# Kernel optimization log

Hardware: AMD Instinct MI355X
Metric: run time of the kernel (lower is better)

## Reference

```python
import jax, jax.numpy as jnp
import numpy as np

B, CIN, COUT, H, W = 4, 64, 64, 64, 64
DI, DS, DR, K = 2 * COUT, 16, COUT // 16, 4   # d_inner, d_state, dt_rank, scan dirs
EPS = 1e-5


def _conv(x, w, b, groups=1):
    y = jax.lax.conv_general_dilated(x, w, (1, 1), 'SAME', feature_group_count=groups,
                                     dimension_numbers=('NCHW', 'OIHW', 'NCHW'))
    return y + b[None, :, None, None]


def _inorm(x):  # InstanceNorm2d, no affine
    m = x.mean(axis=(2, 3), keepdims=True)
    v = x.var(axis=(2, 3), keepdims=True)
    return (x - m) * jax.lax.rsqrt(v + EPS)


def _lrelu(x):
    return jnp.where(x >= 0, x, 0.2 * x)


def _ln(x, g, b):
    m = x.mean(-1, keepdims=True)
    v = x.var(-1, keepdims=True)
    return (x - m) * jax.lax.rsqrt(v + EPS) * g + b


def _ss2d(x, in_proj_w, dw_w, dw_b, x_proj_w, dt_proj_w, dt_proj_b,
          A_logs, Ds, out_norm_g, out_norm_b, out_proj_w):
    # x: (b, h, w, c)
    b, h, w, c = x.shape
    L = h * w
    xz = jnp.einsum('bhwc,ec->bhwe', x, in_proj_w)      # (b,h,w,2*DI)
    xin, z = jnp.split(xz, 2, axis=-1)
    xin = xin.transpose(0, 3, 1, 2)                      # (b,DI,h,w)
    xin = _conv(xin, dw_w, dw_b, groups=DI)              # depthwise 3x3
    xin = jax.nn.silu(xin)
    # 4-direction scans: row-major, col-major, and their reverses
    x_hw = xin.reshape(b, DI, L)
    x_wh = xin.transpose(0, 1, 3, 2).reshape(b, DI, L)
    xs = jnp.stack([x_hw, x_wh, jnp.flip(x_hw, -1), jnp.flip(x_wh, -1)], axis=1)  # (b,K,DI,L)
    x_dbl = jnp.einsum('bkdl,kcd->bkcl', xs, x_proj_w)   # c = DR + 2*DS
    dts, Bs, Cs = jnp.split(x_dbl, [DR, DR + DS], axis=2)
    dt = jax.nn.softplus(jnp.einsum('bkrl,kdr->bkdl', dts, dt_proj_w)
                         + dt_proj_b[None, :, :, None])  # (b,K,DI,L)
    A = -jnp.exp(A_logs)                                  # (K,DI,DS)

    def step(hst, inp):
        dt_t, B_t, C_t, u_t = inp  # (b,K,DI),(b,K,DS),(b,K,DS),(b,K,DI)
        hst = hst * jnp.exp(dt_t[..., None] * A[None]) + (dt_t * u_t)[..., None] * B_t[:, :, None, :]
        y = jnp.einsum('bkdn,bkn->bkd', hst, C_t)
        return hst, y

    h0 = jnp.zeros((b, K, DI, DS), xs.dtype)
    scan_in = (dt.transpose(3, 0, 1, 2), Bs.transpose(3, 0, 1, 2),
               Cs.transpose(3, 0, 1, 2), xs.transpose(3, 0, 1, 2))
    _, ys = jax.lax.scan(step, h0, scan_in)               # (L,b,K,DI)
    ys = ys.transpose(1, 2, 3, 0) + Ds[None, :, :, None] * xs  # (b,K,DI,L)
    # undo the 4 traversal orders and sum
    y0 = ys[:, 0]
    y1 = ys[:, 1].reshape(b, DI, w, h).transpose(0, 1, 3, 2).reshape(b, DI, L)
    y2 = jnp.flip(ys[:, 2], -1)
    y3 = jnp.flip(ys[:, 3], -1).reshape(b, DI, w, h).transpose(0, 1, 3, 2).reshape(b, DI, L)
    y = (y0 + y1 + y2 + y3).transpose(0, 2, 1)            # (b,L,DI)
    y = _ln(y, out_norm_g, out_norm_b)
    y = y * jax.nn.silu(z.reshape(b, L, DI))
    out = jnp.einsum('bld,cd->blc', y, out_proj_w)        # (b,L,c)
    return out.reshape(b, h, w, c)


def _mamba(x, cf_w, cf_b, ln_g, ln_b, in_proj_w, dw_w, dw_b, x_proj_w,
           dt_proj_w, dt_proj_b, A_logs, Ds, out_norm_g, out_norm_b,
           out_proj_w, skip_scale, cb_w, cb_b):
    x1 = _conv(x, cf_w, cf_b)                 # shallow feature conv
    xs = x1.transpose(0, 2, 3, 1)             # (b,h,w,c)
    xs = xs * skip_scale + _ss2d(_ln(xs, ln_g, ln_b), in_proj_w, dw_w, dw_b,
                                 x_proj_w, dt_proj_w, dt_proj_b, A_logs, Ds,
                                 out_norm_g, out_norm_b, out_proj_w)
    res = xs.transpose(0, 3, 1, 2)
    return _conv(res, cb_w, cb_b) + x1        # conv_after_body + residual


def reference(x, conv1_w, conv1_b, conv2_w, conv2_b, cf_w, cf_b, ln_g, ln_b,
              in_proj_w, dw_w, dw_b, x_proj_w, dt_proj_w, dt_proj_b, A_logs,
              Ds, out_norm_g, out_norm_b, out_proj_w, skip_scale, cb_w, cb_b):
    out = _lrelu(_inorm(_conv(x, conv1_w, conv1_b)))
    out = _conv(out, conv2_w, conv2_b)
    out = _mamba(out, cf_w, cf_b, ln_g, ln_b, in_proj_w, dw_w, dw_b, x_proj_w,
                 dt_proj_w, dt_proj_b, A_logs, Ds, out_norm_g, out_norm_b,
                 out_proj_w, skip_scale, cb_w, cb_b)
    return _lrelu(_inorm(out))


def setup_inputs() -> dict:
    key = jax.random.key(0)
    ks = jax.random.split(key, 12)
    n = lambda k, shape, scale: jax.random.normal(k, shape, jnp.float32) * scale
    p = {}
    p['x'] = jax.random.normal(ks[0], (B, CIN, H, W), jnp.float32)
    p['conv1_w'] = n(ks[1], (COUT, CIN, 3, 3), (CIN * 9) ** -0.5)
    p['conv1_b'] = jnp.zeros((COUT,))
    p['conv2_w'] = n(ks[2], (COUT, COUT, 3, 3), (COUT * 9) ** -0.5)
    p['conv2_b'] = jnp.zeros((COUT,))
    p['cf_w'] = n(ks[3], (COUT, COUT, 3, 3), (COUT * 9) ** -0.5)
    p['cf_b'] = jnp.zeros((COUT,))
    p['ln_g'] = jnp.ones((COUT,))
    p['ln_b'] = jnp.zeros((COUT,))
    p['in_proj_w'] = n(ks[4], (2 * DI, COUT), COUT ** -0.5)
    p['dw_w'] = n(ks[5], (DI, 1, 3, 3), 1.0 / 3.0)
    p['dw_b'] = jnp.zeros((DI,))
    p['x_proj_w'] = n(ks[6], (K, DR + 2 * DS, DI), DI ** -0.5)
    p['dt_proj_w'] = n(ks[7], (K, DI, DR), DR ** -0.5)
    p['dt_proj_b'] = jnp.full((K, DI), float(np.log(np.expm1(0.01))), jnp.float32)
    p['A_logs'] = jnp.log(jnp.tile(jnp.arange(1., DS + 1., dtype=jnp.float32), (K, DI, 1)))
    p['Ds'] = jnp.ones((K, DI))
    p['out_norm_g'] = jnp.ones((DI,))
    p['out_norm_b'] = jnp.zeros((DI,))
    p['out_proj_w'] = n(ks[8], (COUT, DI), DI ** -0.5)
    p['skip_scale'] = jnp.ones(())
    p['cb_w'] = n(ks[9], (COUT, COUT, 3, 3), (COUT * 9) ** -0.5)
    p['cb_b'] = jnp.zeros((COUT,))
    return p
```

## Files before the change

kernel.cpp:

```cpp
#include <hip/hip_runtime.h>
#include <hip/hip_bf16.h>


typedef __attribute__((ext_vector_type(8))) short bf16x8;
typedef __attribute__((ext_vector_type(8))) unsigned short u16x8;
typedef __attribute__((ext_vector_type(4))) float f32x4;
typedef unsigned short u16;

static __device__ __forceinline__ short f2bf(float f)
{
    unsigned u = __float_as_uint(f);
    unsigned r = u + 0x7FFFu + ((u >> 16) & 1u);
    return (short)(r >> 16);
}
static __device__ __forceinline__ float b2f(u16 s)
{
    return __uint_as_float((unsigned)s << 16);
}

static __device__ __forceinline__ float softplus_f(float s)
{
    return (s > 15.f) ? s : __logf(1.f + __expf(s));
}

static __device__ __forceinline__ float dpp_sum16(float x)
{
    x += __int_as_float(__builtin_amdgcn_update_dpp(
        0, __float_as_int(x), 0xB1, 0xF, 0xF, true));
    x += __int_as_float(__builtin_amdgcn_update_dpp(
        0, __float_as_int(x), 0x4E, 0xF, 0xF, true));
    x += __int_as_float(__builtin_amdgcn_update_dpp(
        0, __float_as_int(x), 0x141, 0xF, 0xF, true));
    x += __int_as_float(__builtin_amdgcn_update_dpp(
        0, __float_as_int(x), 0x140, 0xF, 0xF, true));
    return x;
}

__global__ __launch_bounds__(256) void wconv_k(const float* __restrict__ w1,
    const float* __restrict__ w2, const float* __restrict__ w3,
    const float* __restrict__ w4, const float* __restrict__ ipw,
    const float* __restrict__ xpw, short* __restrict__ wbf,
    short* __restrict__ wxp)
{
    const int idx = blockIdx.x * 256 + threadIdx.x;
    if (idx < 147456) {
        const int c = idx / 36864, rem = idx % 36864;
        const int tap = rem >> 12, r2 = rem & 4095;
        const int co = r2 >> 6, ci = r2 & 63;
        const float* src = (c == 0) ? w1 : (c == 1) ? w2 : (c == 2) ? w3 : w4;
        wbf[idx] = f2bf(src[(co * 64 + ci) * 9 + tap]);
    } else if (idx < 163840) {
        const int i2 = idx - 147456;
        wbf[idx] = f2bf(ipw[i2]);
    } else {
        const int i3 = idx - 163840;
        const int src = i3 / 10240, r = i3 % 10240;
        const int cc = r >> 7, dd = r & 127;
        float v = 0.f;
        if (cc < 72) {
            const int k = src + ((cc >= 36) ? 2 : 0);
            const int c = (cc >= 36) ? (cc - 36) : cc;
            v = xpw[((size_t)(k * 36 + c)) * 128 + dd];
        }
        wxp[i3] = f2bf(v);
    }
}

__global__ __launch_bounds__(256) void conv3x3_mfma_k(const float* __restrict__ in,
    const short* __restrict__ wtap, const float* __restrict__ bias,
    const float* __restrict__ addsrc, const float* __restrict__ instats,
    float* __restrict__ outstats, float* __restrict__ out)
{
    const int bh = blockIdx.x;
    const int b = bh >> 6, h = bh & 63;
    const int t = threadIdx.x;
    __shared__ __align__(16) short lin[3 * 66 * 72];
    {
        const int ci = t >> 2, w16 = (t & 3) * 16;
        float mu = 0.f, rstd = 1.f;
        if (instats) {
            const float S1 = instats[(b << 6) + ci];
            const float S2 = instats[256 + (b << 6) + ci];
            mu = S1 * (1.f / 4096.f);
            rstd = rsqrtf(S2 * (1.f / 4096.f) - mu * mu + 1e-5f);
        }
#pragma unroll
        for (int r = 0; r < 3; ++r) {
            const int hh = h - 1 + r;
            const bool ok = (hh >= 0 && hh < 64);
            const float* src = in + ((size_t)(b * 64 + ci) * 64 + (ok ? hh : 0)) * 64 + w16;
#pragma unroll
            for (int q = 0; q < 4; ++q) {
                float4 v = make_float4(0.f, 0.f, 0.f, 0.f);
                if (ok) {
                    v = *(const float4*)(src + q * 4);
                    if (instats) {
#define NRM(E) { float nv = (v.E - mu) * rstd; v.E = (nv >= 0.f) ? nv : 0.2f * nv; }
                        NRM(x) NRM(y) NRM(z) NRM(w)
#undef NRM
                    }
                }
                const int wb = w16 + q * 4;
                lin[(r * 66 + wb + 1) * 72 + ci] = f2bf(v.x);
                lin[(r * 66 + wb + 2) * 72 + ci] = f2bf(v.y);
                lin[(r * 66 + wb + 3) * 72 + ci] = f2bf(v.z);
                lin[(r * 66 + wb + 4) * 72 + ci] = f2bf(v.w);
            }
        }
        if (t < 216) {
            const int r3 = t / 72, rem = t % 72;
            const int colp = (rem >= 36) ? 65 : 0, ci2 = rem % 36;
            ((int*)lin)[(r3 * 66 + colp) * 36 + ci2] = 0;
        }
    }
    __syncthreads();
    const int lane = t & 63, ct = t >> 6;
    const int n16 = lane & 15, quad = lane >> 4;
    f32x4 acc0 = {0.f, 0.f, 0.f, 0.f};
    f32x4 acc1 = {0.f, 0.f, 0.f, 0.f};
    f32x4 acc2 = {0.f, 0.f, 0.f, 0.f};
    f32x4 acc3 = {0.f, 0.f, 0.f, 0.f};
#pragma unroll
    for (int tap = 0; tap < 9; ++tap) {
        const int dy = tap / 3, dx = tap % 3;
#pragma unroll
        for (int kh = 0; kh < 2; ++kh) {
            const int kk = kh * 32;
            const bf16x8 a = *(const bf16x8*)(wtap +
                ((size_t)tap * 64 + ct * 16 + n16) * 64 + kk + quad * 8);
            const int rb = (dy * 66 + n16 + dx) * 72 + kk + quad * 8;
            const bf16x8 b0 = *(const bf16x8*)&lin[rb + 0 * 16 * 72];
            const bf16x8 b1 = *(const bf16x8*)&lin[rb + 1 * 16 * 72];
            const bf16x8 b2 = *(const bf16x8*)&lin[rb + 2 * 16 * 72];
            const bf16x8 b3 = *(const bf16x8*)&lin[rb + 3 * 16 * 72];
            acc0 = __builtin_amdgcn_mfma_f32_16x16x32_bf16(a, b0, acc0, 0, 0, 0);
            acc1 = __builtin_amdgcn_mfma_f32_16x16x32_bf16(a, b1, acc1, 0, 0, 0);
            acc2 = __builtin_amdgcn_mfma_f32_16x16x32_bf16(a, b2, acc2, 0, 0, 0);
            acc3 = __builtin_amdgcn_mfma_f32_16x16x32_bf16(a, b3, acc3, 0, 0, 0);
        }
    }
#pragma unroll
    for (int r = 0; r < 4; ++r) {
        const int co = ct * 16 + quad * 4 + r;
        const float bv = bias[co];
        float* orow = out + ((size_t)(b * 64 + co) * 64 + h) * 64;
        float v0 = acc0[r] + bv, v1 = acc1[r] + bv, v2 = acc2[r] + bv, v3 = acc3[r] + bv;
        if (addsrc) {
            const float* arow = addsrc + ((size_t)(b * 64 + co) * 64 + h) * 64;
            v0 += arow[n16]; v1 += arow[16 + n16];
            v2 += arow[32 + n16]; v3 += arow[48 + n16];
        }
        if (outstats) {
            float ss = (v0 + v1) + (v2 + v3);
            float qq = fmaf(v0, v0, fmaf(v1, v1, fmaf(v2, v2, v3 * v3)));
            ss = dpp_sum16(ss);
            qq = dpp_sum16(qq);
            if (n16 == 0) {
                atomicAdd(&outstats[(b << 6) + co], ss);
                atomicAdd(&outstats[256 + (b << 6) + co], qq);
            }
        }
        orow[n16] = v0; orow[16 + n16] = v1;
        orow[32 + n16] = v2; orow[48 + n16] = v3;
    }
}

__global__ __launch_bounds__(256) void inorm_apply_k(const float* __restrict__ in,
    const float* __restrict__ stats, float* __restrict__ out)
{
    const int bc = blockIdx.x;
    const float S1 = stats[bc], S2 = stats[256 + bc];
    const float mu = S1 * (1.f / 4096.f);
    const float rstd = rsqrtf(S2 * (1.f / 4096.f) - mu * mu + 1e-5f);
    const float* row = in + (size_t)bc * 4096;
    float* orow = out + (size_t)bc * 4096;
    for (int i = threadIdx.x; i < 4096; i += 256) {
        float v = (row[i] - mu) * rstd;
        orow[i] = (v >= 0.f) ? v : 0.2f * v;
    }
}

__global__ __launch_bounds__(256) void ln_inproj_mfma_k(const float* __restrict__ x1,
    const float* __restrict__ g, const float* __restrict__ be,
    const short* __restrict__ wip, u16* __restrict__ xinrawD,
    float* __restrict__ z)
{
    const int bx = blockIdx.x;
    const int b = bx >> 7, l0 = (bx & 127) * 32;
    const int t = threadIdx.x;
    __shared__ __align__(16) short ltile[32 * 72];
    __shared__ float ztile[32 * 140];
    __shared__ __align__(16) u16 stile[32 * 136];
    {
        const int j = t & 31, gg = t >> 5;
        float xr[64];
        float s1 = 0.f, s2 = 0.f;
#pragma unroll
        for (int c = 0; c < 64; ++c) {
            const float v = x1[(b * 64 + c) * 4096 + l0 + j];
            xr[c] = v; s1 += v; s2 = fmaf(v, v, s2);
        }
        const float mu = s1 * (1.f / 64.f);
        const float var = s2 * (1.f / 64.f) - mu * mu;
        const float rstd = rsqrtf(var + 1e-5f);
#pragma unroll
        for (int i = 0; i < 8; ++i) {
            const int c = gg * 8 + i;
            ltile[j * 72 + c] = f2bf((xr[c] - mu) * rstd * g[c] + be[c]);
        }
    }
    __syncthreads();
    const int lane = t & 63, wv = t >> 6;
    const int n16 = lane & 15, quad = lane >> 4;
    f32x4 acc[4][2];
#pragma unroll
    for (int i = 0; i < 4; ++i)
#pragma unroll
        for (int p = 0; p < 2; ++p) acc[i][p] = (f32x4){0.f, 0.f, 0.f, 0.f};
#pragma unroll
    for (int i = 0; i < 4; ++i) {
        const int cot = wv * 4 + i;
#pragma unroll
        for (int kh = 0; kh < 2; ++kh) {
            const bf16x8 a = *(const bf16x8*)(wip +
                (size_t)(cot * 16 + n16) * 64 + kh * 32 + quad * 8);
#pragma unroll
            for (int p = 0; p < 2; ++p) {
                const bf16x8 bb = *(const bf16x8*)&ltile[
                    (p * 16 + n16) * 72 + kh * 32 + quad * 8];
                acc[i][p] = __builtin_amdgcn_mfma_f32_16x16x32_bf16(a, bb, acc[i][p], 0, 0, 0);
            }
        }
    }
#pragma unroll
    for (int i = 0; i < 4; ++i) {
        const int cot = wv * 4 + i;
#pragma unroll
        for (int p = 0; p < 2; ++p) {
            const int pos = p * 16 + n16;
#pragma unroll
            for (int r = 0; r < 4; ++r) {
                const int e = cot * 16 + quad * 4 + r;
                const float v = acc[i][p][r];
                if (e < 128) stile[pos * 136 + e] = (u16)f2bf(v);
                else ztile[pos * 140 + (e - 128)] = v;
            }
        }
    }
    __syncthreads();
    {
        const int pos = t >> 3, d0 = (t & 7) * 16;
        float* dst = z + ((size_t)(b * 4096 + l0 + pos)) * 128 + d0;
        const float* srcz = ztile + pos * 140 + d0;
#pragma unroll
        for (int q = 0; q < 4; ++q)
            *(float4*)(dst + q * 4) = *(const float4*)(srcz + q * 4);
        u16* dst2 = xinrawD + ((size_t)(b * 4096 + l0 + pos)) * 128 + d0;
        *(u16x8*)dst2 = *(const u16x8*)&stile[pos * 136 + d0];
        *(u16x8*)(dst2 + 8) = *(const u16x8*)&stile[pos * 136 + d0 + 8];
    }
}

__global__ __launch_bounds__(256) void dwconv_dT_k(const u16* __restrict__ in,
    const float* __restrict__ w, const float* __restrict__ bias,
    u16* __restrict__ xin_sD, u16* __restrict__ xin_TD)
{
    __shared__ float sw[1152];
    __shared__ float sb[128];
    for (int e = threadIdx.x; e < 1152; e += 256) sw[e] = w[e];
    if (threadIdx.x < 128) sb[threadIdx.x] = bias[threadIdx.x];
    __syncthreads();
    const int bx = blockIdx.x;
    const int b = bx >> 9, m0 = (bx & 511) * 8;
    const int t = threadIdx.x;
    const int d = t & 127, mloc = t >> 7;
    const u16* base = in + (size_t)b * 4096 * 128 + d;
    const float* wd = sw + d * 9;
    const float bv = sb[d];
#pragma unroll
    for (int i = 0; i < 4; ++i) {
        const int m = m0 + mloc + i * 2;
        const int hh = m >> 6, ww = m & 63;
        float acc = bv;
        const bool hm = hh > 0, hp = hh < 63, wm = ww > 0, wp = ww < 63;
        if (hm) {
            const u16* r = base + (m - 64) * 128;
            if (wm) acc = fmaf(b2f(r[-128]), wd[0], acc);
            acc = fmaf(b2f(r[0]), wd[1], acc);
            if (wp) acc = fmaf(b2f(r[128]), wd[2], acc);
        }
        {
            const u16* r = base + m * 128;
            if (wm) acc = fmaf(b2f(r[-128]), wd[3], acc);
            acc = fmaf(b2f(r[0]), wd[4], acc);
            if (wp) acc = fmaf(b2f(r[128]), wd[5], acc);
        }
        if (hp) {
            const u16* r = base + (m + 64) * 128;
            if (wm) acc = fmaf(b2f(r[-128]), wd[6], acc);
            acc = fmaf(b2f(r[0]), wd[7], acc);
            if (wp) acc = fmaf(b2f(r[128]), wd[8], acc);
        }
        const float val = acc / (1.f + __expf(-acc));
        const u16 bf = (u16)f2bf(val);
        xin_sD[((size_t)b * 4096 + m) * 128 + d] = bf;
        xin_TD[((size_t)b * 4096 + (ww * 64 + hh)) * 128 + d] = bf;
    }
}

__global__ __launch_bounds__(256) void xdbl_mfma_k(const u16* __restrict__ xin_sD,
    const u16* __restrict__ xin_TD, const short* __restrict__ wxp,
    float* __restrict__ xdbl_mc)
{
    const int bx = blockIdx.x;
    const int tile = bx & 63, src = (bx >> 6) & 1, b = bx >> 7;
    const int m0 = tile * 64;
    const int t = threadIdx.x;
    const int wv = t >> 6, lane = t & 63;
    const int n16 = lane & 15, quad = lane >> 4;
    const u16* srcp = (src ? xin_TD : xin_sD) + (size_t)b * 4096 * 128;
    const short* wb = wxp + (size_t)src * 80 * 128;
    f32x4 acc[5];
#pragma unroll
    for (int c = 0; c < 5; ++c) acc[c] = (f32x4){0.f, 0.f, 0.f, 0.f};
    const u16* brow = srcp + (size_t)(m0 + wv * 16 + n16) * 128 + quad * 8;
#pragma unroll
    for (int kc = 0; kc < 4; ++kc) {
        const bf16x8 bfrag = *(const bf16x8*)(brow + kc * 32);
#pragma unroll
        for (int ct = 0; ct < 5; ++ct) {
            const bf16x8 afrag = *(const bf16x8*)(wb +
                (size_t)(ct * 16 + n16) * 128 + kc * 32 + quad * 8);
            acc[ct] = __builtin_amdgcn_mfma_f32_16x16x32_bf16(afrag, bfrag, acc[ct], 0, 0, 0);
        }
    }
    __shared__ float sres[64 * 81];
#pragma unroll
    for (int ct = 0; ct < 5; ++ct)
#pragma unroll
        for (int r = 0; r < 4; ++r)
            sres[(wv * 16 + n16) * 81 + ct * 16 + quad * 4 + r] = acc[ct][r];
    __syncthreads();
    float* outp = xdbl_mc + ((size_t)(b * 2 + src) * 4096 + m0) * 72;
    for (int e = t; e < 4608; e += 256) {
        const int mm = e / 72, cc = e - mm * 72;
        outp[e] = sres[mm * 81 + cc];
    }
}

__global__ __launch_bounds__(256) void scan_p1_k(const float* __restrict__ xdbl_mc,
    const u16* __restrict__ xin_sD, const u16* __restrict__ xin_TD,
    const float* __restrict__ dtw, const float* __restrict__ dtb,
    float* __restrict__ hseg, float* __restrict__ pseg)
{
    const int bx = blockIdx.x;
    const int bk = bx >> 6;
    const int t = threadIdx.x;
    const int d = t & 127;
    const int seg = __builtin_amdgcn_readfirstlane((bx & 63) * 2 + (t >> 7));
    const int b = bk >> 2, k = bk & 3;
    const bool rev = (k >= 2);
    const u16* srcu = ((k & 1) ? xin_TD : xin_sD) + (size_t)b * 4096 * 128 + d;
    const int m0 = seg * 32;
    const float* xb = xdbl_mc + (size_t)(b * 2 + (k & 1)) * 4096 * 72
                      + (rev ? 36 : 0);
    const float* wpt = dtw + (k * 128 + d) * 4;
    const float w0 = wpt[0], w1 = wpt[1], w2 = wpt[2], w3 = wpt[3];
    const float bv = dtb[k * 128 + d];
    float h[16];
#pragma unroll
    for (int n = 0; n < 16; ++n) h[n] = 0.f;
    float S = 0.f;
#pragma unroll 2
    for (int j = 0; j < 32; ++j) {
        const int um = rev ? (4095 - (m0 + j)) : (m0 + j);
        const float* row = xb + (size_t)um * 72;
        float s = bv;
        s = fmaf(row[0], w0, s); s = fmaf(row[1], w1, s);
        s = fmaf(row[2], w2, s); s = fmaf(row[3], w3, s);
        const float sp = softplus_f(s);
        S += sp;
        const float du = sp * b2f(srcu[(size_t)um * 128]);
        const float a1 = __expf(-sp);
        const float a2 = a1 * a1, a3 = a2 * a1, a4 = a2 * a2;
        const float a8 = a4 * a4, a12 = a8 * a4;
        float pw[16];
        pw[0] = a1; pw[1] = a2; pw[2] = a3; pw[3] = a4;
#pragma unroll
        for (int n = 0; n < 4; ++n) {
            pw[4 + n]  = pw[n] * a4;
            pw[8 + n]  = pw[n] * a8;
            pw[12 + n] = pw[n] * a12;
        }
#pragma unroll
        for (int n = 0; n < 16; ++n)
            h[n] = fmaf(h[n], pw[n], du * row[4 + n]);
    }
    const size_t idx = (size_t)seg * 32768 + ((size_t)(bk * 128 + d)) * 16;
    const float pb = __expf(-S);
    const float pb2 = pb * pb, pb3 = pb2 * pb, pb4 = pb2 * pb2;
    const float pb8 = pb4 * pb4, pb12 = pb8 * pb4;
    float pv[16];
    pv[0] = pb; pv[1] = pb2; pv[2] = pb3; pv[3] = pb4;
#pragma unroll
    for (int n = 0; n < 4; ++n) {
        pv[4 + n]  = pv[n] * pb4;
        pv[8 + n]  = pv[n] * pb8;
        pv[12 + n] = pv[n] * pb12;
    }
#pragma unroll
    for (int n4 = 0; n4 < 4; ++n4) {
        *(float4*)&hseg[idx + n4 * 4] =
            make_float4(h[n4 * 4], h[n4 * 4 + 1], h[n4 * 4 + 2], h[n4 * 4 + 3]);
        *(float4*)&pseg[idx + n4 * 4] =
            make_float4(pv[n4 * 4], pv[n4 * 4 + 1], pv[n4 * 4 + 2], pv[n4 * 4 + 3]);
    }
}

__global__ __launch_bounds__(256) void scan_combine_k(const float* __restrict__ hseg,
                                                      float* __restrict__ pseg)
{
    const int i = blockIdx.x * 256 + threadIdx.x;
    float h = 0.f;
#pragma unroll 8
    for (int s = 0; s < 128; ++s) {
        const size_t idx = (size_t)s * 32768 + i;
        const float p = pseg[idx];
        const float he = hseg[idx];
        pseg[idx] = h;
        h = fmaf(h, p, he);
    }
}

__global__ __launch_bounds__(256) void scan_p2_k(const float* __restrict__ xdbl_mc,
    const u16* __restrict__ xin_sD, const u16* __restrict__ xin_TD,
    const float* __restrict__ dtw, const float* __restrict__ dtb,
    const float* __restrict__ hstart, const float* __restrict__ Dsp,
    u16* __restrict__ ybuf)
{
    const int bx = blockIdx.x;
    const int bk = bx >> 6;
    const int t = threadIdx.x;
    const int d = t & 127;
    const int seg = __builtin_amdgcn_readfirstlane((bx & 63) * 2 + (t >> 7));
    const int b = bk >> 2, k = bk & 3;
    const bool rev = (k >= 2);
    const u16* srcu = ((k & 1) ? xin_TD : xin_sD) + (size_t)b * 4096 * 128 + d;
    const int m0 = seg * 32;
    const float* xb = xdbl_mc + (size_t)(b * 2 + (k & 1)) * 4096 * 72
                      + (rev ? 36 : 0);
    const float* wpt = dtw + (k * 128 + d) * 4;
    const float w0 = wpt[0], w1 = wpt[1], w2 = wpt[2], w3 = wpt[3];
    const float bv = dtb[k * 128 + d];
    const float Dk0 = (k == 0)
        ? (Dsp[d] + Dsp[128 + d] + Dsp[256 + d] + Dsp[384 + d]) : 0.f;
    const size_t idx = (size_t)seg * 32768 + ((size_t)(bk * 128 + d)) * 16;
    float h[16];
#pragma unroll
    for (int n4 = 0; n4 < 4; ++n4) {
        const float4 hv = *(const float4*)&hstart[idx + n4 * 4];
        h[n4 * 4] = hv.x; h[n4 * 4 + 1] = hv.y;
        h[n4 * 4 + 2] = hv.z; h[n4 * 4 + 3] = hv.w;
    }
    u16* yk = ybuf + (size_t)(k * 4 + b) * 4096 * 128 + d;
#pragma unroll 2
    for (int j = 0; j < 32; ++j) {
        const int m = m0 + j;
        const int um = rev ? (4095 - m) : m;
        const float* row = xb + (size_t)um * 72;
        float s = bv;
        s = fmaf(row[0], w0, s); s = fmaf(row[1], w1, s);
        s = fmaf(row[2], w2, s); s = fmaf(row[3], w3, s);
        const float sp = softplus_f(s);
        const float u = b2f(srcu[(size_t)um * 128]);
        const float du = sp * u;
        const float a1 = __expf(-sp);
        const float a2 = a1 * a1, a3 = a2 * a1, a4 = a2 * a2;
        const float a8 = a4 * a4, a12 = a8 * a4;
        float pw[16];
        pw[0] = a1; pw[1] = a2; pw[2] = a3; pw[3] = a4;
#pragma unroll
        for (int n = 0; n < 4; ++n) {
            pw[4 + n]  = pw[n] * a4;
            pw[8 + n]  = pw[n] * a8;
            pw[12 + n] = pw[n] * a12;
        }
        float y0 = Dk0 * u, y1 = 0.f, y2 = 0.f, y3 = 0.f;
#pragma unroll
        for (int n4 = 0; n4 < 4; ++n4) {
            h[n4 * 4 + 0] = fmaf(h[n4 * 4 + 0], pw[n4 * 4 + 0], du * row[4 + n4 * 4 + 0]);
            h[n4 * 4 + 1] = fmaf(h[n4 * 4 + 1], pw[n4 * 4 + 1], du * row[4 + n4 * 4 + 1]);
            h[n4 * 4 + 2] = fmaf(h[n4 * 4 + 2], pw[n4 * 4 + 2], du * row[4 + n4 * 4 + 2]);
            h[n4 * 4 + 3] = fmaf(h[n4 * 4 + 3], pw[n4 * 4 + 3], du * row[4 + n4 * 4 + 3]);
            y0 = fmaf(h[n4 * 4 + 0], row[20 + n4 * 4 + 0], y0);
            y1 = fmaf(h[n4 * 4 + 1], row[20 + n4 * 4 + 1], y1);
            y2 = fmaf(h[n4 * 4 + 2], row[20 + n4 * 4 + 2], y2);
            y3 = fmaf(h[n4 * 4 + 3], row[20 + n4 * 4 + 3], y3);
        }
        const float y = (y0 + y1) + (y2 + y3);
        int l;
        if (k == 0) l = m;
        else if (k == 1) l = ((m & 63) << 6) | (m >> 6);
        else if (k == 2) l = 4095 - m;
        else { const int mf = 4095 - m; l = ((mf & 63) << 6) | (mf >> 6); }
        yk[(size_t)l * 128] = (u16)f2bf(y);
    }
}

__global__ __launch_bounds__(256) void finalize_k(const u16* __restrict__ ybuf,
    const float* __restrict__ z, const float* __restrict__ x1,
    const float* __restrict__ ong, const float* __restrict__ onb,
    const float* __restrict__ opw, const float* __restrict__ skipp,
    float* __restrict__ res)
{
    const int bx = blockIdx.x;
    const int b = bx >> 7, l0 = (bx & 127) * 32;
    const int t = threadIdx.x;
    const int j = t & 31, g = t >> 5;
    const int l = l0 + j;
    const u16x8* y0p = (const u16x8*)(ybuf + ((size_t)(0 + b) * 4096 + l) * 128);
    const u16x8* y1p = (const u16x8*)(ybuf + ((size_t)(4 + b) * 4096 + l) * 128);
    const u16x8* y2p = (const u16x8*)(ybuf + ((size_t)(8 + b) * 4096 + l) * 128);
    const u16x8* y3p = (const u16x8*)(ybuf + ((size_t)(12 + b) * 4096 + l) * 128);
    float vr[128];
    float s1 = 0.f, s2 = 0.f;
#pragma unroll
    for (int g8 = 0; g8 < 16; ++g8) {
        const u16x8 a0 = y0p[g8], a1 = y1p[g8], a2 = y2p[g8], a3 = y3p[g8];
#pragma unroll
        for (int e = 0; e < 8; ++e) {
            const float f = (b2f(a0[e]) + b2f(a1[e])) + (b2f(a2[e]) + b2f(a3[e]));
            vr[g8 * 8 + e] = f;
            s1 += f; s2 = fmaf(f, f, s2);
        }
    }
    const float mu = s1 * (1.f / 128.f);
    const float var = s2 * (1.f / 128.f) - mu * mu;
    const float rstd = rsqrtf(var + 1e-5f);
    const float4* zp = (const float4*)(z + ((size_t)(b * 4096 + l)) * 128);
    const float4* gp = (const float4*)ong;
    const float4* bp = (const float4*)onb;
#pragma unroll
    for (int d4 = 0; d4 < 32; ++d4) {
        const float4 gg = gp[d4], bb = bp[d4], zz = zp[d4];
#define GATE(E, IDX)                                                          \
        {                                                                     \
            const float yln = (vr[d4 * 4 + IDX] - mu) * rstd * gg.E + bb.E;   \
            vr[d4 * 4 + IDX] = yln * (zz.E / (1.f + __expf(-zz.E)));          \
        }
        GATE(x, 0) GATE(y, 1) GATE(z, 2) GATE(w, 3)
#undef GATE
    }
    float acc[8] = {0.f, 0.f, 0.f, 0.f, 0.f, 0.f, 0.f, 0.f};
    for (int d4 = 0; d4 < 32; ++d4) {
#pragma unroll
        for (int q = 0; q < 8; ++q) {
            const float4 wv = *(const float4*)&opw[(size_t)(g * 8 + q) * 128 + d4 * 4];
            acc[q] = fmaf(vr[d4 * 4 + 0], wv.x, acc[q]);
            acc[q] = fmaf(vr[d4 * 4 + 1], wv.y, acc[q]);
            acc[q] = fmaf(vr[d4 * 4 + 2], wv.z, acc[q]);
            acc[q] = fmaf(vr[d4 * 4 + 3], wv.w, acc[q]);
        }
    }
    __shared__ float sres[64 * 33];
#pragma unroll
    for (int q = 0; q < 8; ++q) sres[(g * 8 + q) * 33 + j] = acc[q];
    __syncthreads();
    const float sk = skipp[0];
    for (int e = t; e < 2048; e += 256) {
        const int co = e >> 5, jj = e & 31;
        const size_t o = ((size_t)(b * 64 + co)) * 4096 + l0 + jj;
        res[o] = sres[co * 33 + jj] + sk * x1[o];
    }
}

extern "C" void kernel_launch(void* const* d_in, const int* in_sizes, int n_in,
                              void* d_out, int out_size, void* d_ws, size_t ws_size,
                              hipStream_t stream)
{
    const float* x          = (const float*)d_in[0];
    const float* conv1_w    = (const float*)d_in[1];
    const float* conv1_b    = (const float*)d_in[2];
    const float* conv2_w    = (const float*)d_in[3];
    const float* conv2_b    = (const float*)d_in[4];
    const float* cf_w       = (const float*)d_in[5];
    const float* cf_b       = (const float*)d_in[6];
    const float* ln_g       = (const float*)d_in[7];
    const float* ln_b       = (const float*)d_in[8];
    const float* in_proj_w  = (const float*)d_in[9];
    const float* dw_w       = (const float*)d_in[10];
    const float* dw_b       = (const float*)d_in[11];
    const float* x_proj_w   = (const float*)d_in[12];
    const float* dt_proj_w  = (const float*)d_in[13];
    const float* dt_proj_b  = (const float*)d_in[14];
    const float* Ds         = (const float*)d_in[16];
    const float* out_norm_g = (const float*)d_in[17];
    const float* out_norm_b = (const float*)d_in[18];
    const float* out_proj_w = (const float*)d_in[19];
    const float* skip_scale = (const float*)d_in[20];
    const float* cb_w       = (const float*)d_in[21];
    const float* cb_b       = (const float*)d_in[22];

    float* ws = (float*)d_ws;
    float* x1    = ws;
    u16* xin_sD  = (u16*)(ws + 1048576);
    float* zbuf  = ws + 3145728;
    u16* xin_TD  = (u16*)(ws + 5242880);
    float* xdbl  = ws + 7340032;
    u16* ybuf    = (u16*)(ws + 9699328);
    float* hseg  = ws + 9699328;
    float* pseg  = ws + 13893632;
    short* wxp   = (short*)(ws + 13893632);
    float* G     = ws + 18087936;
    float* G0 = G;
    float* G1 = G + 1048576;
    u16* xinrawD = (u16*)G0;
    short* wbf  = (short*)(ws + 20185088);
    short* wbf1 = wbf;
    short* wbf2 = wbf + 36864;
    short* wbf3 = wbf + 73728;
    short* wbf4 = wbf + 110592;
    short* wip  = wbf + 147456;
    float* stats1 = ws + 20267008;
    float* stats2 = ws + 20267520;

    hipMemsetAsync(stats1, 0, 1024 * sizeof(float), stream);

    wconv_k<<<720, 256, 0, stream>>>(conv1_w, conv2_w, cf_w, cb_w, in_proj_w,
                                     x_proj_w, wbf, wxp);

    conv3x3_mfma_k<<<256, 256, 0, stream>>>(x, wbf1, conv1_b, nullptr,
                                            nullptr, stats1, G0);
    conv3x3_mfma_k<<<256, 256, 0, stream>>>(G0, wbf2, conv2_b, nullptr,
                                            stats1, nullptr, G1);
    conv3x3_mfma_k<<<256, 256, 0, stream>>>(G1, wbf3, cf_b, nullptr,
                                            nullptr, nullptr, x1);
    ln_inproj_mfma_k<<<512, 256, 0, stream>>>(x1, ln_g, ln_b, wip, xinrawD, zbuf);
    dwconv_dT_k<<<2048, 256, 0, stream>>>(xinrawD, dw_w, dw_b, xin_sD, xin_TD);
    xdbl_mfma_k<<<512, 256, 0, stream>>>(xin_sD, xin_TD, wxp, xdbl);
    scan_p1_k<<<1024, 256, 0, stream>>>(xdbl, xin_sD, xin_TD, dt_proj_w,
                                        dt_proj_b, hseg, pseg);
    scan_combine_k<<<128, 256, 0, stream>>>(hseg, pseg );
    scan_p2_k<<<1024, 256, 0, stream>>>(xdbl, xin_sD, xin_TD, dt_proj_w,
                                        dt_proj_b, pseg , Ds, ybuf);
    finalize_k<<<512, 256, 0, stream>>>(ybuf, zbuf, x1, out_norm_g, out_norm_b,
                                        out_proj_w, skip_scale, G0 );
    conv3x3_mfma_k<<<256, 256, 0, stream>>>(G0 , wbf4, cb_b, x1,
                                            nullptr, stats2, G1 );
    inorm_apply_k<<<256, 256, 0, stream>>>(G1 , stats2, (float*)d_out);
}
```

Measured before the change: 296.7 us.

## Pass conv intermediates as bf16 NHWC between the first three convs and LN

Adds a conv3x3 variant that stages its output tile in shared memory and writes it as bf16 NHWC. Conv2, conv3 and the LayerNorm/in_proj kernel then read vectorised, channel-contiguous rows instead of strided fp32 NCHW, with the LN channel reduction done by a DPP sum across 8 lanes. This cuts the global traffic and the transposed scalar LDS writes on the front of the pipeline. Separately, the final instance-norm apply is split over four times as many blocks for more parallelism. The intermediates are now rounded to bf16 before the next stage, and conv3 still writes an fp32 NCHW copy for the skip path.

```diff
diff --git a/kernel.cpp b/kernel.cpp
--- a/kernel.cpp
+++ b/kernel.cpp
@@ -33,6 +33,17 @@
         0, __float_as_int(x), 0x141, 0xF, 0xF, true));
     x += __int_as_float(__builtin_amdgcn_update_dpp(
         0, __float_as_int(x), 0x140, 0xF, 0xF, true));
+    return x;
+}
+
+static __device__ __forceinline__ float dpp_sum8(float x)
+{
+    x += __int_as_float(__builtin_amdgcn_update_dpp(
+        0, __float_as_int(x), 0xB1, 0xF, 0xF, true));
+    x += __int_as_float(__builtin_amdgcn_update_dpp(
+        0, __float_as_int(x), 0x4E, 0xF, 0xF, true));
+    x += __int_as_float(__builtin_amdgcn_update_dpp(
+        0, __float_as_int(x), 0x141, 0xF, 0xF, true));
     return x;
 }
 
@@ -66,6 +77,140 @@
     }
 }
 
+__global__ __launch_bounds__(256) void conv3x3_nhwc_k(const void* __restrict__ inptr,
+    const int in_bf16, const short* __restrict__ wtap, const float* __restrict__ bias,
+    const float* __restrict__ instats, float* __restrict__ outstats,
+    u16* __restrict__ out_nhwc, float* __restrict__ out_nchw)
+{
+    const int bh = blockIdx.x;
+    const int b = bh >> 6, h = bh & 63;
+    const int t = threadIdx.x;
+    __shared__ __align__(16) short lin[3 * 66 * 72];
+    __shared__ __align__(16) u16 sout[64 * 72];
+    if (in_bf16) {
+        const u16* in2 = (const u16*)inptr;
+        const int wloc = t >> 3, ci0 = (t & 7) * 8;
+        float mu8[8], rs8[8];
+        if (instats) {
+#pragma unroll
+            for (int e = 0; e < 8; ++e) {
+                const float S1 = instats[(b << 6) + ci0 + e];
+                const float S2 = instats[256 + (b << 6) + ci0 + e];
+                const float mu = S1 * (1.f / 4096.f);
+                mu8[e] = mu;
+                rs8[e] = rsqrtf(S2 * (1.f / 4096.f) - mu * mu + 1e-5f);
+            }
+        }
+#pragma unroll
+        for (int r = 0; r < 3; ++r) {
+            const int hh = h - 1 + r;
+            const bool ok = (hh >= 0 && hh < 64);
+#pragma unroll
+            for (int p = 0; p < 2; ++p) {
+                const int w = wloc + p * 32;
+                u16x8 v = (u16x8){0, 0, 0, 0, 0, 0, 0, 0};
+                if (ok) v = *(const u16x8*)(in2 +
+                        ((size_t)(b * 4096 + hh * 64 + w)) * 64 + ci0);
+                if (instats) {
+                    bf16x8 st;
+#pragma unroll
+                    for (int e = 0; e < 8; ++e) {
+                        float f = (b2f(v[e]) - mu8[e]) * rs8[e];
+                        f = (f >= 0.f) ? f : 0.2f * f;
+                        st[e] = f2bf(f);
+                    }
+                    *(bf16x8*)&lin[(r * 66 + w + 1) * 72 + ci0] = st;
+                } else {
+                    *(u16x8*)&lin[(r * 66 + w + 1) * 72 + ci0] = v;
+                }
+            }
+        }
+    } else {
+        const float* in = (const float*)inptr;
+        const int ci = t >> 2, w16 = (t & 3) * 16;
+#pragma unroll
+        for (int r = 0; r < 3; ++r) {
+            const int hh = h - 1 + r;
+            const bool ok = (hh >= 0 && hh < 64);
+            const float* src = in + ((size_t)(b * 64 + ci) * 64 + (ok ? hh : 0)) * 64 + w16;
+#pragma unroll
+            for (int q = 0; q < 4; ++q) {
+                float4 v = make_float4(0.f, 0.f, 0.f, 0.f);
+                if (ok) v = *(const float4*)(src + q * 4);
+                const int wb = w16 + q * 4;
+                lin[(r * 66 + wb + 1) * 72 + ci] = f2bf(v.x);
+                lin[(r * 66 + wb + 2) * 72 + ci] = f2bf(v.y);
+                lin[(r * 66 + wb + 3) * 72 + ci] = f2bf(v.z);
+                lin[(r * 66 + wb + 4) * 72 + ci] = f2bf(v.w);
+            }
+        }
+    }
+    if (t < 216) {
+        const int r3 = t / 72, rem = t % 72;
+        const int colp = (rem >= 36) ? 65 : 0, ci2 = rem % 36;
+        ((int*)lin)[(r3 * 66 + colp) * 36 + ci2] = 0;
+    }
+    __syncthreads();
+    const int lane = t & 63, ct = t >> 6;
+    const int n16 = lane & 15, quad = lane >> 4;
+    f32x4 acc0 = {0.f, 0.f, 0.f, 0.f};
+    f32x4 acc1 = {0.f, 0.f, 0.f, 0.f};
+    f32x4 acc2 = {0.f, 0.f, 0.f, 0.f};
+    f32x4 acc3 = {0.f, 0.f, 0.f, 0.f};
+#pragma unroll
+    for (int tap = 0; tap < 9; ++tap) {
+        const int dy = tap / 3, dx = tap % 3;
+#pragma unroll
+        for (int kh = 0; kh < 2; ++kh) {
+            const int kk = kh * 32;
+            const bf16x8 a = *(const bf16x8*)(wtap +
+                ((size_t)tap * 64 + ct * 16 + n16) * 64 + kk + quad * 8);
+            const int rb = (dy * 66 + n16 + dx) * 72 + kk + quad * 8;
+            const bf16x8 b0 = *(const bf16x8*)&lin[rb + 0 * 16 * 72];
+            const bf16x8 b1 = *(const bf16x8*)&lin[rb + 1 * 16 * 72];
+            const bf16x8 b2 = *(const bf16x8*)&lin[rb + 2 * 16 * 72];
+            const bf16x8 b3 = *(const bf16x8*)&lin[rb + 3 * 16 * 72];
+            acc0 = __builtin_amdgcn_mfma_f32_16x16x32_bf16(a, b0, acc0, 0, 0, 0);
+            acc1 = __builtin_amdgcn_mfma_f32_16x16x32_bf16(a, b1, acc1, 0, 0, 0);
+            acc2 = __builtin_amdgcn_mfma_f32_16x16x32_bf16(a, b2, acc2, 0, 0, 0);
+            acc3 = __builtin_amdgcn_mfma_f32_16x16x32_bf16(a, b3, acc3, 0, 0, 0);
+        }
+    }
+#pragma unroll
+    for (int r = 0; r < 4; ++r) {
+        const int co = ct * 16 + quad * 4 + r;
+        const float bv = bias[co];
+        const float v0 = acc0[r] + bv, v1 = acc1[r] + bv;
+        const float v2 = acc2[r] + bv, v3 = acc3[r] + bv;
+        if (outstats) {
+            float ss = (v0 + v1) + (v2 + v3);
+            float qq = fmaf(v0, v0, fmaf(v1, v1, fmaf(v2, v2, v3 * v3)));
+            ss = dpp_sum16(ss);
+            qq = dpp_sum16(qq);
+            if (n16 == 0) {
+                atomicAdd(&outstats[(b << 6) + co], ss);
+                atomicAdd(&outstats[256 + (b << 6) + co], qq);
+            }
+        }
+        if (out_nchw) {
+            float* orow = out_nchw + ((size_t)(b * 64 + co) * 64 + h) * 64;
+            orow[n16] = v0; orow[16 + n16] = v1;
+            orow[32 + n16] = v2; orow[48 + n16] = v3;
+        }
+        sout[(n16 +  0) * 72 + co] = (u16)f2bf(v0);
+        sout[(n16 + 16) * 72 + co] = (u16)f2bf(v1);
+        sout[(n16 + 32) * 72 + co] = (u16)f2bf(v2);
+        sout[(n16 + 48) * 72 + co] = (u16)f2bf(v3);
+    }
+    if (out_nhwc) {
+        __syncthreads();
+        u16* orow = out_nhwc + ((size_t)(b * 4096 + h * 64)) * 64;
+        const int w = t >> 2, ci0 = (t & 3) * 16;
+        *(u16x8*)(orow + w * 64 + ci0) = *(u16x8*)&sout[w * 72 + ci0];
+        *(u16x8*)(orow + w * 64 + ci0 + 8) = *(u16x8*)&sout[w * 72 + ci0 + 8];
+    }
+}
+
 __global__ __launch_bounds__(256) void conv3x3_mfma_k(const float* __restrict__ in,
     const short* __restrict__ wtap, const float* __restrict__ bias,
     const float* __restrict__ addsrc, const float* __restrict__ instats,
@@ -168,19 +313,19 @@
 __global__ __launch_bounds__(256) void inorm_apply_k(const float* __restrict__ in,
     const float* __restrict__ stats, float* __restrict__ out)
 {
-    const int bc = blockIdx.x;
+    const int bc = blockIdx.x >> 2, qo = (blockIdx.x & 3) * 1024;
     const float S1 = stats[bc], S2 = stats[256 + bc];
     const float mu = S1 * (1.f / 4096.f);
     const float rstd = rsqrtf(S2 * (1.f / 4096.f) - mu * mu + 1e-5f);
-    const float* row = in + (size_t)bc * 4096;
-    float* orow = out + (size_t)bc * 4096;
-    for (int i = threadIdx.x; i < 4096; i += 256) {
+    const float* row = in + (size_t)bc * 4096 + qo;
+    float* orow = out + (size_t)bc * 4096 + qo;
+    for (int i = threadIdx.x; i < 1024; i += 256) {
         float v = (row[i] - mu) * rstd;
         orow[i] = (v >= 0.f) ? v : 0.2f * v;
     }
 }
 
-__global__ __launch_bounds__(256) void ln_inproj_mfma_k(const float* __restrict__ x1,
+__global__ __launch_bounds__(256) void ln_inproj_mfma_k(const u16* __restrict__ x1bf,
     const float* __restrict__ g, const float* __restrict__ be,
     const short* __restrict__ wip, u16* __restrict__ xinrawD,
     float* __restrict__ z)
@@ -192,22 +337,28 @@
     __shared__ float ztile[32 * 140];
     __shared__ __align__(16) u16 stile[32 * 136];
     {
-        const int j = t & 31, gg = t >> 5;
-        float xr[64];
+        const int j = t >> 3, gg = t & 7;
+        const int l = l0 + j;
+        const u16x8 v = *(const u16x8*)(x1bf + ((size_t)(b * 4096 + l)) * 64 + gg * 8);
+        float f[8];
         float s1 = 0.f, s2 = 0.f;
 #pragma unroll
-        for (int c = 0; c < 64; ++c) {
-            const float v = x1[(b * 64 + c) * 4096 + l0 + j];
-            xr[c] = v; s1 += v; s2 = fmaf(v, v, s2);
-        }
+        for (int e = 0; e < 8; ++e) {
+            f[e] = b2f(v[e]);
+            s1 += f[e]; s2 = fmaf(f[e], f[e], s2);
+        }
+        s1 = dpp_sum8(s1);
+        s2 = dpp_sum8(s2);
         const float mu = s1 * (1.f / 64.f);
         const float var = s2 * (1.f / 64.f) - mu * mu;
         const float rstd = rsqrtf(var + 1e-5f);
-#pragma unroll
-        for (int i = 0; i < 8; ++i) {
-            const int c = gg * 8 + i;
-            ltile[j * 72 + c] = f2bf((xr[c] - mu) * rstd * g[c] + be[c]);
-        }
+        bf16x8 st;
+#pragma unroll
+        for (int e = 0; e < 8; ++e) {
+            const int c = gg * 8 + e;
+            st[e] = f2bf((f[e] - mu) * rstd * g[c] + be[c]);
+        }
+        *(bf16x8*)&ltile[j * 72 + gg * 8] = st;
     }
     __syncthreads();
     const int lane = t & 63, wv = t >> 6;
@@ -623,19 +774,22 @@
     short* wip  = wbf + 147456;
     float* stats1 = ws + 20267008;
     float* stats2 = ws + 20267520;
+    u16* G0bf    = (u16*)(ws + 20268032);
+    u16* G1bf    = (u16*)(ws + 20792320);
+    u16* x1bf    = (u16*)(ws + 21316608);
 
     hipMemsetAsync(stats1, 0, 1024 * sizeof(float), stream);
 
     wconv_k<<<720, 256, 0, stream>>>(conv1_w, conv2_w, cf_w, cb_w, in_proj_w,
                                      x_proj_w, wbf, wxp);
 
-    conv3x3_mfma_k<<<256, 256, 0, stream>>>(x, wbf1, conv1_b, nullptr,
-                                            nullptr, stats1, G0);
-    conv3x3_mfma_k<<<256, 256, 0, stream>>>(G0, wbf2, conv2_b, nullptr,
-                                            stats1, nullptr, G1);
-    conv3x3_mfma_k<<<256, 256, 0, stream>>>(G1, wbf3, cf_b, nullptr,
-                                            nullptr, nullptr, x1);
-    ln_inproj_mfma_k<<<512, 256, 0, stream>>>(x1, ln_g, ln_b, wip, xinrawD, zbuf);
+    conv3x3_nhwc_k<<<256, 256, 0, stream>>>(x, 0, wbf1, conv1_b,
+                                            nullptr, stats1, G0bf, nullptr);
+    conv3x3_nhwc_k<<<256, 256, 0, stream>>>(G0bf, 1, wbf2, conv2_b,
+                                            stats1, nullptr, G1bf, nullptr);
+    conv3x3_nhwc_k<<<256, 256, 0, stream>>>(G1bf, 1, wbf3, cf_b,
+                                            nullptr, nullptr, x1bf, x1);
+    ln_inproj_mfma_k<<<512, 256, 0, stream>>>(x1bf, ln_g, ln_b, wip, xinrawD, zbuf);
     dwconv_dT_k<<<2048, 256, 0, stream>>>(xinrawD, dw_w, dw_b, xin_sD, xin_TD);
     xdbl_mfma_k<<<512, 256, 0, stream>>>(xin_sD, xin_TD, wxp, xdbl);
     scan_p1_k<<<1024, 256, 0, stream>>>(xdbl, xin_sD, xin_TD, dt_proj_w,
@@ -647,5 +801,5 @@
                                         out_proj_w, skip_scale, G0 );
     conv3x3_mfma_k<<<256, 256, 0, stream>>>(G0 , wbf4, cb_b, x1,
                                             nullptr, stats2, G1 );
-    inorm_apply_k<<<256, 256, 0, stream>>>(G1 , stats2, (float*)d_out);
-}
+    inorm_apply_k<<<1024, 256, 0, stream>>>(G1 , stats2, (float*)d_out);
+}
```

After: 282.9 us. -4.7%, faster.
